# Performance work log

Hardware: AMD Instinct MI355X
Metric: run time of the kernel (lower is better)

The kernel has to match this reference:

```python
import jax, jax.numpy as jnp
import numpy as np

DIM = 16        # lagrangian.dim -> y has 2*DIM phase-space coords
HID = 128       # hidden width of the parametric Lagrangian
BATCH = 32768


def setup_inputs() -> dict:
    key = jax.random.key(0)
    k1, k2, k3, k4 = jax.random.split(key, 4)
    y = jax.random.normal(k1, (BATCH, 2 * DIM), dtype=jnp.float32)
    # small-scale init keeps J_{qdot,qdot} = I + (MLP Hessian block) well conditioned
    W1 = jax.random.normal(k2, (HID, 2 * DIM), dtype=jnp.float32) * (1.0 / np.sqrt(2 * DIM))
    b1 = jax.random.normal(k3, (HID,), dtype=jnp.float32) * 0.1
    w2 = jax.random.normal(k4, (HID,), dtype=jnp.float32) * 0.1
    return {"y": y, "W1": W1, "b1": b1, "w2": w2}


def _lagrangian(y_vec, W1, b1, w2):
    """Scalar Lagrangian L(q, qdot) for a single phase-space vector y_vec [2*DIM]."""
    qdot = y_vec[DIM:]
    kinetic = 0.5 * jnp.dot(qdot, qdot)
    return kinetic + jnp.dot(w2, jnp.tanh(W1 @ y_vec + b1))


def reference(y, W1, b1, w2):
    """Acceleration qdotdot = (dL/dq - qdot . J_{q,qdot}) . J_{qdot,qdot}^{-1}.

    Instead of the original O(dim^2) repeated tf.gradients calls, compute the
    full gradient and Hessian once per sample via fused forward-over-reverse
    autodiff, vmapped over the batch.
    """
    d = DIM
    L = lambda yv: _lagrangian(yv, W1, b1, w2)
    grad_fn = jax.grad(L)
    hess_fn = jax.jacfwd(grad_fn)  # forward-over-reverse Hessian, one sweep

    g = jax.vmap(grad_fn)(y)   # [B, 2d]   full dL/dy
    H = jax.vmap(hess_fn)(y)   # [B, 2d, 2d]  full Hessian d2L/(dy dy)

    qdot = y[:, d:]            # [B, d]
    dLdq = g[:, :d]            # [B, d]
    J_qqdot = H[:, :d, d:]     # [B, d, d]  d2L/(dq_i dqdot_j)
    J_qdqd_inv = jnp.linalg.inv(H[:, d:, d:])  # [B, d, d]

    rhs = dLdq - jnp.einsum('bi,bij->bj', qdot, J_qqdot)
    qdotdot = jnp.einsum('bi,bij->bj', rhs, J_qdqd_inv)
    return qdotdot
```

## Files before the change

### kernel.cpp

```cpp
#include <hip/hip_runtime.h>
#include <math.h>

#define DIMQ 16
#define HID  128
#define SPB  32
#define NTHREADS 512

typedef __attribute__((ext_vector_type(8))) _Float16 f16x8;
typedef __attribute__((ext_vector_type(4))) _Float16 f16x4;
typedef __attribute__((ext_vector_type(4))) float f32x4;

#define ASTR 280
#define USTR 280
#define SSTR 136

#define OFF_WBF  0
#define OFF_YBF  8192
#define OFF_ABT  10240
#define OFF_USP  19200
#define OFF_SST  37120
#define OFF_B1   45824
#define OFF_W2   46336
#define OFF_MSCR 0
#define LDS_BYTES 46848

__device__ __forceinline__ int mswz(int s, int off) {
    return s * 320 + (off ^ ((s & 7) << 2));
}

__global__ __launch_bounds__(NTHREADS, 4)
void lag_accel_kernel(const float* __restrict__ y,
                      const float* __restrict__ W1,
                      const float* __restrict__ b1,
                      const float* __restrict__ w2,
                      float* __restrict__ out)
{
    __shared__ __align__(16) char smem[LDS_BYTES];
    _Float16* Wbf = (_Float16*)(smem + OFF_WBF);
    _Float16* Ybf = (_Float16*)(smem + OFF_YBF);
    _Float16* ABT = (_Float16*)(smem + OFF_ABT);
    _Float16* usp = (_Float16*)(smem + OFF_USP);
    _Float16* sst = (_Float16*)(smem + OFF_SST);
    float* b1s = (float*)(smem + OFF_B1);
    float* w2s = (float*)(smem + OFF_W2);

    const int tid = threadIdx.x;
    const long long s0 = (long long)blockIdx.x * SPB;

    for (int idx = tid; idx < HID * 32; idx += NTHREADS) {
        float v = W1[idx];
        int h = idx >> 5, k = idx & 31;
        _Float16 hv = (_Float16)v;
        Wbf[h * 32 + k] = hv;
        if (k < 16) ABT[k * ASTR + h] = hv;
        else        ABT[(k - 16) * ASTR + 128 + h] = hv;
    }
    for (int idx = tid; idx < SPB * 32; idx += NTHREADS)
        Ybf[idx] = (_Float16)y[s0 * 32 + idx];
    if (tid < HID) { b1s[tid] = b1[tid]; w2s[tid] = w2[tid]; }

    const int wave = tid >> 6;
    const int lane = tid & 63;
    const int grp  = lane >> 4;
    const int j    = lane & 15;
    const int ht   = wave;

    __syncthreads();

    f16x8 aW  = *(const f16x8*)&Wbf[(ht * 16 + j) * 32 + (grp << 3)];
    f16x8 aAl = *(const f16x8*)&Wbf[(ht * 16 + j) * 32 + ((grp & 1) << 3)];
    f16x8 aA;
#pragma unroll
    for (int e = 0; e < 8; ++e) aA[e] = (grp >= 2) ? aAl[e] : (_Float16)0.0f;

    float4 b1v = *(const float4*)&b1s[ht * 16 + (grp << 2)];
    float4 w2v = *(const float4*)&w2s[ht * 16 + (grp << 2)];

    f32x4 zacc[2], aacc[2];
    {
        f32x4 ci; ci[0] = b1v.x; ci[1] = b1v.y; ci[2] = b1v.z; ci[3] = b1v.w;
        f32x4 zf = {0.0f, 0.0f, 0.0f, 0.0f};
        f16x8 yf0 = *(const f16x8*)&Ybf[(0 * 16 + j) * 32 + (grp << 3)];
        f16x8 yf1 = *(const f16x8*)&Ybf[(1 * 16 + j) * 32 + (grp << 3)];
        zacc[0] = __builtin_amdgcn_mfma_f32_16x16x32_f16(aW, yf0, ci, 0, 0, 0);
        zacc[1] = __builtin_amdgcn_mfma_f32_16x16x32_f16(aW, yf1, ci, 0, 0, 0);
        aacc[0] = __builtin_amdgcn_mfma_f32_16x16x32_f16(aA, yf0, zf, 0, 0, 0);
        aacc[1] = __builtin_amdgcn_mfma_f32_16x16x32_f16(aA, yf1, zf, 0, 0, 0);
    }

    const int h4 = ht * 16 + (grp << 2);
#define EWST(st)                                                         \
    {                                                                    \
        _Float16 su[4], sn[4], sv[4];                                    \
        _Pragma("unroll")                                                \
        for (int r = 0; r < 4; ++r) {                                    \
            float z  = zacc[st][r], aq = aacc[st][r];                    \
            float w2c = (r == 0) ? w2v.x : (r == 1) ? w2v.y               \
                       : (r == 2) ? w2v.z : w2v.w;                       \
            float e  = __expf(2.0f * z);                                 \
            float rr = 2.0f * __builtin_amdgcn_rcpf(e + 1.0f);           \
            float t  = 1.0f - rr;                                        \
            float u  = w2c * (rr * (2.0f - rr));                         \
            float s  = -2.0f * t * u;                                    \
            float sp = s * aq;                                           \
            su[r] = (_Float16)u; sn[r] = (_Float16)(-sp);                \
            sv[r] = (_Float16)s;                                         \
        }                                                                \
        const int smp2 = (st) * 16 + j;                                  \
        f16x4 pa = {su[0], su[1], su[2], su[3]};                         \
        f16x4 pb = {sn[0], sn[1], sn[2], sn[3]};                         \
        f16x4 pc = {sv[0], sv[1], sv[2], sv[3]};                         \
        *(f16x4*)&usp[smp2 * USTR + h4]       = pa;                      \
        *(f16x4*)&usp[smp2 * USTR + 128 + h4] = pb;                      \
        *(f16x4*)&sst[smp2 * SSTR + h4]       = pc;                      \
    }
    EWST(0)
    EWST(1)
#undef EWST

    __syncthreads();

    f32x4 racc = {0.0f, 0.0f, 0.0f, 0.0f};
    if (wave < 2) {
#pragma unroll
        for (int kc = 0; kc < 8; ++kc) {
            f16x8 af = *(const f16x8*)&ABT[j * ASTR + (kc << 5) + (grp << 3)];
            f16x8 bf = *(const f16x8*)&usp[(wave * 16 + j) * USTR + (kc << 5) + (grp << 3)];
            racc = __builtin_amdgcn_mfma_f32_16x16x32_f16(af, bf, racc, 0, 0, 0);
        }
    }

    f32x4 acc[4];
    {
        f32x4 ident;
#pragma unroll
        for (int r = 0; r < 4; ++r) ident[r] = ((grp << 2) + r == j) ? 1.0f : 0.0f;
#pragma unroll
        for (int gs = 0; gs < 4; ++gs) acc[gs] = ident;
    }
#pragma unroll
    for (int kc = 0; kc < 4; ++kc) {
        f16x8 bfrag = *(const f16x8*)&ABT[j * ASTR + 128 + (kc << 5) + (grp << 3)];
#pragma unroll
        for (int gs = 0; gs < 4; ++gs) {
            f16x8 sfrag = *(const f16x8*)&sst[(wave * 4 + gs) * SSTR + (kc << 5) + (grp << 3)];
            f16x8 afrag = sfrag * bfrag;
            acc[gs] = __builtin_amdgcn_mfma_f32_16x16x32_f16(afrag, bfrag, acc[gs], 0, 0, 0);
        }
    }

    __syncthreads();

    float* Mscr = (float*)(smem + OFF_MSCR);
#pragma unroll
    for (int gs = 0; gs < 4; ++gs) {
        float4 v;
        v.x = acc[gs][0]; v.y = acc[gs][1]; v.z = acc[gs][2]; v.w = acc[gs][3];
        *(float4*)&Mscr[mswz(wave * 4 + gs, j * 20 + (grp << 2))] = v;
    }

    __syncthreads();

    if (wave >= 2) return;
    const int sl = lane & 15;
    const int rb = lane >> 4;
    const int s  = wave * 16 + sl;

    float M4[4][16], r4[4], d4[4];
#pragma unroll
    for (int r = 0; r < 4; ++r) {
        const int ro = (4 * rb + r) * 20;
        float4 v0 = *(const float4*)&Mscr[mswz(s, ro + 0)];
        float4 v1 = *(const float4*)&Mscr[mswz(s, ro + 4)];
        float4 v2 = *(const float4*)&Mscr[mswz(s, ro + 8)];
        float4 v3 = *(const float4*)&Mscr[mswz(s, ro + 12)];
        M4[r][0]=v0.x; M4[r][1]=v0.y; M4[r][2]=v0.z; M4[r][3]=v0.w;
        M4[r][4]=v1.x; M4[r][5]=v1.y; M4[r][6]=v1.z; M4[r][7]=v1.w;
        M4[r][8]=v2.x; M4[r][9]=v2.y; M4[r][10]=v2.z; M4[r][11]=v2.w;
        M4[r][12]=v3.x; M4[r][13]=v3.y; M4[r][14]=v3.z; M4[r][15]=v3.w;
        r4[r] = racc[r];
        d4[r] = 1.0f;
    }

#pragma unroll
    for (int k = 0; k < 16; ++k) {
        const int src = sl + ((k >> 2) << 4);
        float piv = __shfl(M4[k & 3][k], src, 64);
        float rk  = __shfl(r4[k & 3], src, 64);
        float invp = __builtin_amdgcn_rcpf(piv);
        invp = invp * (2.0f - piv * invp);
        float f[4];
#pragma unroll
        for (int r = 0; r < 4; ++r) {
            float fr = M4[r][k] * invp;
            const bool isk = ((rb << 2) + r) == k;
            f[r]  = isk ? 0.0f : fr;
            d4[r] = isk ? piv : d4[r];
            r4[r] = fmaf(-f[r], rk, r4[r]);
        }
#pragma unroll
        for (int i = k + 1; i < 16; ++i) {
            float p = __shfl(M4[k & 3][i], src, 64);
            M4[0][i] = fmaf(-f[0], p, M4[0][i]);
            M4[1][i] = fmaf(-f[1], p, M4[1][i]);
            M4[2][i] = fmaf(-f[2], p, M4[2][i]);
            M4[3][i] = fmaf(-f[3], p, M4[3][i]);
        }
    }

    float4 xo;
    {
        float i0 = __builtin_amdgcn_rcpf(d4[0]); i0 = i0 * (2.0f - d4[0] * i0);
        float i1 = __builtin_amdgcn_rcpf(d4[1]); i1 = i1 * (2.0f - d4[1] * i1);
        float i2 = __builtin_amdgcn_rcpf(d4[2]); i2 = i2 * (2.0f - d4[2] * i2);
        float i3 = __builtin_amdgcn_rcpf(d4[3]); i3 = i3 * (2.0f - d4[3] * i3);
        xo.x = r4[0] * i0; xo.y = r4[1] * i1; xo.z = r4[2] * i2; xo.w = r4[3] * i3;
    }
    *(float4*)&out[(s0 + s) * DIMQ + (rb << 2)] = xo;
}

extern "C" void kernel_launch(void* const* d_in, const int* in_sizes, int n_in,
                              void* d_out, int out_size, void* d_ws, size_t ws_size,
                              hipStream_t stream) {
    const float* y  = (const float*)d_in[0];
    const float* W1 = (const float*)d_in[1];
    const float* b1 = (const float*)d_in[2];
    const float* w2 = (const float*)d_in[3];
    float* out = (float*)d_out;
    const int batch = in_sizes[0] / 32;
    const int blocks = (batch + SPB - 1) / SPB;
    lag_accel_kernel<<<blocks, NTHREADS, 0, stream>>>(y, W1, b1, w2, out);
}
```

Measured before the change: 20.28 us.

## Precompute fp16 W1 fragment layouts in a prep kernel and read them from global

A small prep kernel converts W1 to fp16 once and writes both a row-major copy and an MFMA-fragment-ordered transposed copy into workspace. The main kernel then loads its weight fragments straight from global memory (L2-resident) and reads b1/w2 directly, instead of every block converting W1 into LDS. This drops per-block conversion work and LDS use, which may allow more blocks per CU. The cost is a second kernel launch and global/L2 fragment loads inside the MFMA loops in place of LDS reads.

```diff
diff --git a/kernel.cpp b/kernel.cpp
--- a/kernel.cpp
+++ b/kernel.cpp
@@ -10,54 +10,57 @@
 typedef __attribute__((ext_vector_type(4))) _Float16 f16x4;
 typedef __attribute__((ext_vector_type(4))) float f32x4;
 
-#define ASTR 280
 #define USTR 280
 #define SSTR 136
 
-#define OFF_WBF  0
-#define OFF_YBF  8192
-#define OFF_ABT  10240
-#define OFF_USP  19200
-#define OFF_SST  37120
-#define OFF_B1   45824
-#define OFF_W2   46336
+#define OFF_YBF  0
+#define OFF_USP  2048
+#define OFF_SST  19968
 #define OFF_MSCR 0
-#define LDS_BYTES 46848
+#define LDS_BYTES 40960
 
 __device__ __forceinline__ int mswz(int s, int off) {
     return s * 320 + (off ^ ((s & 7) << 2));
 }
 
+__global__ void lag_prep_kernel(const float* __restrict__ W1,
+                                _Float16* __restrict__ wsp)
+{
+    const int idx = blockIdx.x * 256 + threadIdx.x;
+    const float v = W1[idx];
+    const _Float16 hv = (_Float16)v;
+    _Float16* Wh = wsp;
+    _Float16* G  = wsp + 4096;
+    const int h = idx >> 5, k = idx & 31;
+    Wh[idx] = hv;
+    const int kc  = h >> 5;
+    const int grp = (h >> 3) & 3;
+    const int e   = h & 7;
+    const int j   = (k < 16) ? k : (k - 16);
+    const int kk  = (k < 16) ? kc : (kc + 4);
+    G[((kk * 4 + grp) * 16 + j) * 8 + e] = hv;
+}
+
 __global__ __launch_bounds__(NTHREADS, 4)
 void lag_accel_kernel(const float* __restrict__ y,
-                      const float* __restrict__ W1,
+                      const _Float16* __restrict__ wsp,
                       const float* __restrict__ b1,
                       const float* __restrict__ w2,
                       float* __restrict__ out)
 {
     __shared__ __align__(16) char smem[LDS_BYTES];
-    _Float16* Wbf = (_Float16*)(smem + OFF_WBF);
     _Float16* Ybf = (_Float16*)(smem + OFF_YBF);
-    _Float16* ABT = (_Float16*)(smem + OFF_ABT);
     _Float16* usp = (_Float16*)(smem + OFF_USP);
     _Float16* sst = (_Float16*)(smem + OFF_SST);
-    float* b1s = (float*)(smem + OFF_B1);
-    float* w2s = (float*)(smem + OFF_W2);
+
+    const f16x8* Wh8 = (const f16x8*)wsp;
+    const f16x8* G8  = (const f16x8*)(wsp + 4096);
 
     const int tid = threadIdx.x;
     const long long s0 = (long long)blockIdx.x * SPB;
 
-    for (int idx = tid; idx < HID * 32; idx += NTHREADS) {
-        float v = W1[idx];
-        int h = idx >> 5, k = idx & 31;
-        _Float16 hv = (_Float16)v;
-        Wbf[h * 32 + k] = hv;
-        if (k < 16) ABT[k * ASTR + h] = hv;
-        else        ABT[(k - 16) * ASTR + 128 + h] = hv;
-    }
     for (int idx = tid; idx < SPB * 32; idx += NTHREADS)
         Ybf[idx] = (_Float16)y[s0 * 32 + idx];
-    if (tid < HID) { b1s[tid] = b1[tid]; w2s[tid] = w2[tid]; }
 
     const int wave = tid >> 6;
     const int lane = tid & 63;
@@ -65,16 +68,15 @@
     const int j    = lane & 15;
     const int ht   = wave;
 
-    __syncthreads();
-
-    f16x8 aW  = *(const f16x8*)&Wbf[(ht * 16 + j) * 32 + (grp << 3)];
-    f16x8 aAl = *(const f16x8*)&Wbf[(ht * 16 + j) * 32 + ((grp & 1) << 3)];
+    f16x8 aW  = Wh8[(ht * 16 + j) * 4 + grp];
+    f16x8 aAl = Wh8[(ht * 16 + j) * 4 + (grp & 1)];
     f16x8 aA;
 #pragma unroll
     for (int e = 0; e < 8; ++e) aA[e] = (grp >= 2) ? aAl[e] : (_Float16)0.0f;
-
-    float4 b1v = *(const float4*)&b1s[ht * 16 + (grp << 2)];
-    float4 w2v = *(const float4*)&w2s[ht * 16 + (grp << 2)];
+    float4 b1v = *(const float4*)&b1[ht * 16 + (grp << 2)];
+    float4 w2v = *(const float4*)&w2[ht * 16 + (grp << 2)];
+
+    __syncthreads();
 
     f32x4 zacc[2], aacc[2];
     {
@@ -124,7 +126,7 @@
     if (wave < 2) {
 #pragma unroll
         for (int kc = 0; kc < 8; ++kc) {
-            f16x8 af = *(const f16x8*)&ABT[j * ASTR + (kc << 5) + (grp << 3)];
+            f16x8 af = G8[(kc * 4 + grp) * 16 + j];
             f16x8 bf = *(const f16x8*)&usp[(wave * 16 + j) * USTR + (kc << 5) + (grp << 3)];
             racc = __builtin_amdgcn_mfma_f32_16x16x32_f16(af, bf, racc, 0, 0, 0);
         }
@@ -140,7 +142,7 @@
     }
 #pragma unroll
     for (int kc = 0; kc < 4; ++kc) {
-        f16x8 bfrag = *(const f16x8*)&ABT[j * ASTR + 128 + (kc << 5) + (grp << 3)];
+        f16x8 bfrag = G8[((kc + 4) * 4 + grp) * 16 + j];
 #pragma unroll
         for (int gs = 0; gs < 4; ++gs) {
             f16x8 sfrag = *(const f16x8*)&sst[(wave * 4 + gs) * SSTR + (kc << 5) + (grp << 3)];
@@ -227,7 +229,9 @@
     const float* b1 = (const float*)d_in[2];
     const float* w2 = (const float*)d_in[3];
     float* out = (float*)d_out;
+    _Float16* wsp = (_Float16*)d_ws;
     const int batch = in_sizes[0] / 32;
     const int blocks = (batch + SPB - 1) / SPB;
-    lag_accel_kernel<<<blocks, NTHREADS, 0, stream>>>(y, W1, b1, w2, out);
-}
+    lag_prep_kernel<<<16, 256, 0, stream>>>(W1, wsp);
+    lag_accel_kernel<<<blocks, NTHREADS, 0, stream>>>(y, wsp, b1, w2, out);
+}
```

Measured after the change: 23.40 us. +15.4%, slower.
